# Kernel optimization log

Measured on AMD Instinct MI355X. Metric: run time of the kernel, lower is better.

Reference implementation:

```python
import jax, jax.numpy as jnp
import numpy as np

COUNT_BINS = 8
BOUND = 3.0
MIN_BIN_WIDTH = 1e-3
MIN_BIN_HEIGHT = 1e-3
MIN_DERIVATIVE = 1e-3
EPS = 1e-6


def _made_masks(D, H1, H2, M):
    indeg = np.arange(1, D + 1)                     # input degrees 1..D
    h1 = np.arange(H1) % (D - 1) + 1                # hidden degrees in [1, D-1]
    h2 = np.arange(H2) % (D - 1) + 1
    outdeg = np.tile(indeg, M)                      # (M*D,), reshape-compatible with (M, D)
    m1 = (h1[:, None] >= indeg[None, :]).astype(np.float32)   # (H1, D)
    m2 = (h2[:, None] >= h1[None, :]).astype(np.float32)      # (H2, H1)
    m3 = (outdeg[:, None] > h2[None, :]).astype(np.float32)   # (M*D, H2)
    return jnp.asarray(m1), jnp.asarray(m2), jnp.asarray(m3)


def _rq_spline_forward(x, w, h, d):
    # x: (B, D); w, h: (B, D, K) simplex weights; d: (B, D, K-1) softplus'd interior derivatives
    K = w.shape[-1]
    left, right = -BOUND, BOUND

    widths = MIN_BIN_WIDTH + (1.0 - MIN_BIN_WIDTH * K) * w
    heights = MIN_BIN_HEIGHT + (1.0 - MIN_BIN_HEIGHT * K) * h
    derivs = MIN_DERIVATIVE + d
    ones = jnp.ones_like(derivs[..., :1])
    derivs = jnp.concatenate([ones, derivs, ones], -1)          # (B, D, K+1), boundary slope 1

    cw = jnp.cumsum(widths, -1)
    edge_l = jnp.full_like(cw[..., :1], left)
    edge_r = jnp.full_like(cw[..., :1], right)
    cumw = jnp.concatenate([edge_l, left + (right - left) * cw[..., :-1], edge_r], -1)  # (B, D, K+1)
    widths = cumw[..., 1:] - cumw[..., :-1]
    ch = jnp.cumsum(heights, -1)
    cumh = jnp.concatenate([edge_l, left + (right - left) * ch[..., :-1], edge_r], -1)
    heights = cumh[..., 1:] - cumh[..., :-1]

    inside = (x >= left) & (x <= right)
    xc = jnp.clip(x, left, right)
    # pyro: bin_idx = sum(x >= cumwidths + eps) - 1
    idx = jnp.sum((xc[..., None] >= (cumw + EPS)).astype(jnp.int32), -1) - 1
    idx = jnp.clip(idx, 0, K - 1)                               # (B, D)

    def g(t):
        return jnp.take_along_axis(t, idx[..., None], axis=-1)[..., 0]

    x_k, w_k = g(cumw), g(widths)
    y_k, h_k = g(cumh), g(heights)
    delta = h_k / w_k
    d_k, d_k1 = g(derivs), g(derivs[..., 1:])

    theta = (xc - x_k) / w_k
    tt = theta * (1.0 - theta)
    num = h_k * (delta * theta ** 2 + d_k * tt)
    den = delta + (d_k + d_k1 - 2.0 * delta) * tt
    y = y_k + num / den
    dnum = delta ** 2 * (d_k1 * theta ** 2 + 2.0 * delta * tt + d_k * (1.0 - theta) ** 2)
    ld = jnp.log(dnum) - 2.0 * jnp.log(den)
    return jnp.where(inside, y, x), jnp.where(inside, ld, jnp.zeros_like(ld))


def _forward(x, W1, b1, W2, b2, W3, b3):
    B, D = x.shape
    H1, H2 = W1.shape[0], W2.shape[0]
    K = COUNT_BINS
    M = 3 * K - 1
    m1, m2, m3 = _made_masks(D, H1, H2, M)
    h1 = jax.nn.relu(x @ (W1 * m1).T + b1)
    h2 = jax.nn.relu(h1 @ (W2 * m2).T + b2)
    p = (h2 @ (W3 * m3).T + b3).reshape(B, M, D)                # (B, 3K-1, D)
    w = jax.nn.softmax(jnp.swapaxes(p[:, :K, :], 1, 2), axis=-1)          # (B, D, K)
    hgt = jax.nn.softmax(jnp.swapaxes(p[:, K:2 * K, :], 1, 2), axis=-1)   # (B, D, K)
    d = jax.nn.softplus(jnp.swapaxes(p[:, 2 * K:, :], 1, 2))              # (B, D, K-1)
    z, ld = _rq_spline_forward(x, w, hgt, d)
    return z, ld.sum(-1)


def setup_inputs() -> dict:
    key = jax.random.key(0)
    ks = jax.random.split(key, 7)
    B, D, H1, H2 = 32768, 64, 64, 32
    M = 3 * COUNT_BINS - 1
    s1, s2, s3 = 1.0 / np.sqrt(D), 1.0 / np.sqrt(H1), 1.0 / np.sqrt(H2)
    return {
        "x": jax.random.normal(ks[0], (B, D), jnp.float32),
        "W1": jax.random.uniform(ks[1], (H1, D), jnp.float32, -s1, s1),
        "b1": jax.random.uniform(ks[2], (H1,), jnp.float32, -s1, s1),
        "W2": jax.random.uniform(ks[3], (H2, H1), jnp.float32, -s2, s2),
        "b2": jax.random.uniform(ks[4], (H2,), jnp.float32, -s2, s2),
        "W3": jax.random.uniform(ks[5], (M * D, H2), jnp.float32, -s3, s3),
        "b3": jax.random.uniform(ks[6], (M * D,), jnp.float32, -s3, s3),
    }


def reference(x, W1, b1, W2, b2, W3, b3):
    return _forward(x, W1, b1, W2, b2, W3, b3)
```

## Files before the change

kernel.cpp:

```cpp
#include <hip/hip_runtime.h>

#define NM 23

typedef short short8 __attribute__((ext_vector_type(8)));
typedef float f32x4 __attribute__((ext_vector_type(4)));

__device__ __forceinline__ float softplus_f(float v) {
  return fmaxf(v, 0.f) + __logf(1.f + __expf(-fabsf(v)));
}

__device__ __forceinline__ float fastrcp(float v) {
  return __builtin_amdgcn_rcpf(v);
}

__device__ __forceinline__ unsigned short bf16_rne(float x) {
  unsigned u = __float_as_uint(x);
  u += 0x7FFFu + ((u >> 16) & 1u);
  return (unsigned short)(u >> 16);
}

__global__ __launch_bounds__(256) void prep_kernel(
    const float* __restrict__ W1, const float* __restrict__ W2,
    const float* __restrict__ W3,
    unsigned short* __restrict__ B1hi, unsigned short* __restrict__ B1lo,
    unsigned short* __restrict__ B2hi, unsigned short* __restrict__ B2lo,
    unsigned short* __restrict__ B3hi, unsigned short* __restrict__ B3lo) {
  const int idx = blockIdx.x * 256 + threadIdx.x;
  const int j = idx & 7, lane = (idx >> 3) & 63;
  const int col = lane & 15, quad = lane >> 4;

  if (idx < 4096) {
    const int rest = idx >> 9, kt = rest & 1, nt = rest >> 1;
    const int k = kt * 32 + quad * 8 + j;
    const int n = nt * 16 + col;
    const float v = ((n % 63) >= k) ? W1[n * 64 + k] : 0.f;
    const unsigned short h = bf16_rne(v);
    B1hi[idx] = h;
    B1lo[idx] = bf16_rne(v - __uint_as_float(((unsigned)h) << 16));
  }
  if (idx < 2048) {
    const int rest = idx >> 9, kt = rest & 1, nt = rest >> 1;
    const int k = kt * 32 + quad * 8 + j;
    const int n = nt * 16 + col;
    const float v = ((k % 63) <= n) ? W2[n * 64 + k] : 0.f;
    const unsigned short h = bf16_rne(v);
    B2hi[idx] = h;
    B2lo[idx] = bf16_rne(v - __uint_as_float(((unsigned)h) << 16));
  }
  if (idx < 92 * 64 * 8) {
    const int nt = idx >> 9;
    const int n = nt * 16 + col;
    const int d = n & 63;
    const int k = quad * 8 + j;
    const float v = (k < d) ? W3[(size_t)n * 32 + k] : 0.f;
    const unsigned short h = bf16_rne(v);
    B3hi[idx] = h;
    B3lo[idx] = bf16_rne(v - __uint_as_float(((unsigned)h) << 16));
  }
}

__device__ __forceinline__ void cvt_hilo(const float* src, short8& hi,
                                         short8& lo) {
  const f32x4 a0 = *reinterpret_cast<const f32x4*>(src);
  const f32x4 a1 = *reinterpret_cast<const f32x4*>(src + 4);
  const float af[8] = {a0.x, a0.y, a0.z, a0.w, a1.x, a1.y, a1.z, a1.w};
  #pragma unroll
  for (int j = 0; j < 8; ++j) {
    const unsigned short h = bf16_rne(af[j]);
    hi[j] = (short)h;
    lo[j] = (short)bf16_rne(af[j] - __uint_as_float(((unsigned)h) << 16));
  }
}

__global__ __launch_bounds__(256, 2) void fused_kernel(
    const float* __restrict__ x,
    const unsigned short* __restrict__ B1hi,
    const unsigned short* __restrict__ B1lo,
    const float* __restrict__ b1,
    const unsigned short* __restrict__ B2hi,
    const unsigned short* __restrict__ B2lo,
    const float* __restrict__ b2,
    const unsigned short* __restrict__ B3hi,
    const unsigned short* __restrict__ B3lo,
    const float* __restrict__ b3,
    float* __restrict__ out, int B) {
  __shared__ float xs[64][68];
  __shared__ float h1s[64][68];
  __shared__ float h2s[64][36];
  __shared__ float b3s[64 * NM];

  const int t = threadIdx.x;
  const int b0 = blockIdx.x * 64;

  #pragma unroll
  for (int u = 0; u < 4; ++u) {
    const int idx = t + u * 256;
    const int rr = idx >> 4, c4 = (idx & 15) * 4;
    const float4 v = *reinterpret_cast<const float4*>(
        x + (size_t)b0 * 64 + (size_t)idx * 4);
    xs[rr][c4 + 0] = v.x; xs[rr][c4 + 1] = v.y;
    xs[rr][c4 + 2] = v.z; xs[rr][c4 + 3] = v.w;
  }
  for (int idx = t; idx < 64 * NM; idx += 256) {
    const int dl = idx / NM, m = idx - dl * NM;
    b3s[idx] = b3[m * 64 + dl];
  }
  __syncthreads();

  const int lane = t & 63;
  const int wv   = __builtin_amdgcn_readfirstlane(t >> 6);
  const int mt   = wv;
  const int col  = lane & 15;
  const int quad = lane >> 4;
  const int arow = mt * 16 + col;

  {
    short8 ahi[2], alo[2];
    #pragma unroll
    for (int kt = 0; kt < 2; ++kt)
      cvt_hilo(&xs[arow][kt * 32 + quad * 8], ahi[kt], alo[kt]);

    #pragma unroll
    for (int nt = 0; nt < 4; ++nt) {
      const float bv = b1[nt * 16 + col];
      f32x4 acc = {bv, bv, bv, bv};
      #pragma unroll
      for (int kt = 0; kt < 2; ++kt) {
        const size_t off = ((size_t)(nt * 2 + kt) * 64 + lane) * 8;
        const short8 bh = *reinterpret_cast<const short8*>(B1hi + off);
        const short8 bl = *reinterpret_cast<const short8*>(B1lo + off);
        acc = __builtin_amdgcn_mfma_f32_16x16x32_bf16(ahi[kt], bh, acc, 0, 0, 0);
        acc = __builtin_amdgcn_mfma_f32_16x16x32_bf16(alo[kt], bh, acc, 0, 0, 0);
        acc = __builtin_amdgcn_mfma_f32_16x16x32_bf16(ahi[kt], bl, acc, 0, 0, 0);
      }
      #pragma unroll
      for (int reg = 0; reg < 4; ++reg)
        h1s[mt * 16 + quad * 4 + reg][nt * 16 + col] = fmaxf(acc[reg], 0.f);
    }
  }

  {
    short8 ahi[2], alo[2];
    #pragma unroll
    for (int kt = 0; kt < 2; ++kt)
      cvt_hilo(&h1s[arow][kt * 32 + quad * 8], ahi[kt], alo[kt]);

    #pragma unroll
    for (int nt = 0; nt < 2; ++nt) {
      const float bv = b2[nt * 16 + col];
      f32x4 acc = {bv, bv, bv, bv};
      #pragma unroll
      for (int kt = 0; kt < 2; ++kt) {
        const size_t off = ((size_t)(nt * 2 + kt) * 64 + lane) * 8;
        const short8 bh = *reinterpret_cast<const short8*>(B2hi + off);
        const short8 bl = *reinterpret_cast<const short8*>(B2lo + off);
        acc = __builtin_amdgcn_mfma_f32_16x16x32_bf16(ahi[kt], bh, acc, 0, 0, 0);
        acc = __builtin_amdgcn_mfma_f32_16x16x32_bf16(alo[kt], bh, acc, 0, 0, 0);
        acc = __builtin_amdgcn_mfma_f32_16x16x32_bf16(ahi[kt], bl, acc, 0, 0, 0);
      }
      #pragma unroll
      for (int reg = 0; reg < 4; ++reg)
        h2s[mt * 16 + quad * 4 + reg][nt * 16 + col] = fmaxf(acc[reg], 0.f);
    }
  }

  short8 ahi, alo;
  cvt_hilo(&h2s[arow][quad * 8], ahi, alo);

  float ldr[4] = {0.f, 0.f, 0.f, 0.f};

  #pragma unroll 1
  for (int jj = 0; jj < 4; ++jj) {
    const int dc = jj;
    const int d  = dc * 16 + col;

    f32x4 acc[NM];
    #pragma unroll
    for (int m = 0; m < NM; ++m) {
      const float bv = b3s[d * NM + m];
      acc[m] = (f32x4){bv, bv, bv, bv};
    }
    #pragma unroll
    for (int m = 0; m < NM; ++m) {
      const int nt = 4 * m + dc;
      const size_t off = ((size_t)nt * 64 + lane) * 8;
      const short8 bh = *reinterpret_cast<const short8*>(B3hi + off);
      const short8 bl = *reinterpret_cast<const short8*>(B3lo + off);
      acc[m] = __builtin_amdgcn_mfma_f32_16x16x32_bf16(ahi, bh, acc[m], 0, 0, 0);
      acc[m] = __builtin_amdgcn_mfma_f32_16x16x32_bf16(alo, bh, acc[m], 0, 0, 0);
      acc[m] = __builtin_amdgcn_mfma_f32_16x16x32_bf16(ahi, bl, acc[m], 0, 0, 0);
    }

    #pragma unroll
    for (int reg = 0; reg < 4; ++reg) {
      const int row = mt * 16 + quad * 4 + reg;

      float p[NM];
      #pragma unroll
      for (int m = 0; m < NM; ++m) p[m] = acc[m][reg];

      const float xv = xs[row][d];
      const float xc = fminf(fmaxf(xv, -3.f), 3.f);

      float ew[8], sw = 0.f;
      #pragma unroll
      for (int k = 0; k < 8; ++k) { ew[k] = __expf(p[k]); sw += ew[k]; }
      const float invw = fastrcp(sw);

      float eh[8], sh = 0.f;
      #pragma unroll
      for (int k = 0; k < 8; ++k) { eh[k] = __expf(p[8 + k]); sh += eh[k]; }
      const float invh = fastrcp(sh);

      const float WSC = 1.0f - 1e-3f * 8.0f;
      float cumw[9], cumh[9];
      cumw[0] = -3.f; cumh[0] = -3.f;
      float cw = 0.f, ch = 0.f;
      #pragma unroll
      for (int k = 0; k < 7; ++k) {
        cw += 1e-3f + WSC * (ew[k] * invw);
        ch += 1e-3f + WSC * (eh[k] * invh);
        cumw[k + 1] = fmaf(6.f, cw, -3.f);
        cumh[k + 1] = fmaf(6.f, ch, -3.f);
      }
      cumw[8] = 3.f; cumh[8] = 3.f;

      float derivs[9];
      derivs[0] = 1.f; derivs[8] = 1.f;
      #pragma unroll
      for (int k = 0; k < 7; ++k) derivs[k + 1] = 1e-3f + softplus_f(p[16 + k]);

      float xk = cumw[0], xk1 = cumw[1];
      float yk = cumh[0], yk1 = cumh[1];
      float dk = derivs[0], dk1 = derivs[1];
      #pragma unroll
      for (int k = 1; k < 8; ++k) {
        const bool s = xc >= cumw[k] + 1e-6f;
        xk  = s ? cumw[k]       : xk;
        xk1 = s ? cumw[k + 1]   : xk1;
        yk  = s ? cumh[k]       : yk;
        yk1 = s ? cumh[k + 1]   : yk1;
        dk  = s ? derivs[k]     : dk;
        dk1 = s ? derivs[k + 1] : dk1;
      }

      const float wk = xk1 - xk, hk = yk1 - yk;
      const float invwk = fastrcp(wk);
      const float delta = hk * invwk;
      const float theta = (xc - xk) * invwk;
      const float omt = 1.f - theta;
      const float tt = theta * omt;
      const float th2 = theta * theta;
      const float num = hk * (delta * th2 + dk * tt);
      const float den = delta + (dk + dk1 - 2.f * delta) * tt;
      const float rden = fastrcp(den);
      const float yv = yk + num * rden;
      const float dnum = delta * delta * (dk1 * th2 + 2.f * delta * tt + dk * omt * omt);
      const float ldv = __logf(dnum * rden * rden);

      const bool inside = (xv >= -3.f) && (xv <= 3.f);
      xs[row][d] = inside ? yv : xv;
      ldr[reg] += inside ? ldv : 0.f;
    }
  }

  #pragma unroll
  for (int mask = 1; mask <= 8; mask <<= 1) {
    #pragma unroll
    for (int reg = 0; reg < 4; ++reg)
      ldr[reg] += __shfl_xor(ldr[reg], mask, 64);
  }
  __syncthreads();

  if (col == 0) {
    #pragma unroll
    for (int reg = 0; reg < 4; ++reg)
      out[(size_t)B * 64 + b0 + mt * 16 + quad * 4 + reg] = ldr[reg];
  }

  #pragma unroll
  for (int u = 0; u < 4; ++u) {
    const int idx = t + u * 256;
    const int rr = idx >> 4, c4 = (idx & 15) * 4;
    const float4 v = make_float4(xs[rr][c4 + 0], xs[rr][c4 + 1],
                                 xs[rr][c4 + 2], xs[rr][c4 + 3]);
    *reinterpret_cast<float4*>(out + (size_t)(b0 + rr) * 64 + c4) = v;
  }
}

extern "C" void kernel_launch(void* const* d_in, const int* in_sizes, int n_in,
                              void* d_out, int out_size, void* d_ws, size_t ws_size,
                              hipStream_t stream) {
  const float* x  = (const float*)d_in[0];
  const float* W1 = (const float*)d_in[1];
  const float* b1 = (const float*)d_in[2];
  const float* W2 = (const float*)d_in[3];
  const float* b2 = (const float*)d_in[4];
  const float* W3 = (const float*)d_in[5];
  const float* b3 = (const float*)d_in[6];
  float* out = (float*)d_out;
  char* ws   = (char*)d_ws;

  unsigned short* B1hi = (unsigned short*)(ws);
  unsigned short* B1lo = (unsigned short*)(ws + 8192);
  unsigned short* B2hi = (unsigned short*)(ws + 16384);
  unsigned short* B2lo = (unsigned short*)(ws + 20480);
  unsigned short* B3hi = (unsigned short*)(ws + 24576);
  unsigned short* B3lo = (unsigned short*)(ws + 118784);

  const int B = in_sizes[0] / 64;

  prep_kernel<<<184, 256, 0, stream>>>(W1, W2, W3, B1hi, B1lo, B2hi, B2lo,
                                       B3hi, B3lo);

  fused_kernel<<<B / 64, 256, 0, stream>>>(
      x, B1hi, B1lo, b1, B2hi, B2lo, b2, B3hi, B3lo, b3, out, B);
}
```

Measured before the change: 118.4 us.

## Split layer-3 MFMA into three phases to cut registers and raise occupancy

Removes the shared-memory staging tile for x and z, reading x straight from global memory and writing z directly with strided scalar stores. The 23-accumulator layer-3 GEMM is split into three phases (widths, heights, derivatives), each followed by its part of the spline math, so far fewer accumulator registers are live at once. The launch bound is raised to 4 blocks per SIMD. Costs: uncoalesced global loads and stores of x/z, a bin-index carried as float, and a select-based derivative gather.

```diff
diff --git a/kernel.cpp b/kernel.cpp
--- a/kernel.cpp
+++ b/kernel.cpp
@@ -72,7 +72,7 @@
   }
 }
 
-__global__ __launch_bounds__(256, 2) void fused_kernel(
+__global__ __launch_bounds__(256, 4) void fused_kernel(
     const float* __restrict__ x,
     const unsigned short* __restrict__ B1hi,
     const unsigned short* __restrict__ B1lo,
@@ -84,7 +84,6 @@
     const unsigned short* __restrict__ B3lo,
     const float* __restrict__ b3,
     float* __restrict__ out, int B) {
-  __shared__ float xs[64][68];
   __shared__ float h1s[64][68];
   __shared__ float h2s[64][36];
   __shared__ float b3s[64 * NM];
@@ -92,15 +91,6 @@
   const int t = threadIdx.x;
   const int b0 = blockIdx.x * 64;
 
-  #pragma unroll
-  for (int u = 0; u < 4; ++u) {
-    const int idx = t + u * 256;
-    const int rr = idx >> 4, c4 = (idx & 15) * 4;
-    const float4 v = *reinterpret_cast<const float4*>(
-        x + (size_t)b0 * 64 + (size_t)idx * 4);
-    xs[rr][c4 + 0] = v.x; xs[rr][c4 + 1] = v.y;
-    xs[rr][c4 + 2] = v.z; xs[rr][c4 + 3] = v.w;
-  }
   for (int idx = t; idx < 64 * NM; idx += 256) {
     const int dl = idx / NM, m = idx - dl * NM;
     b3s[idx] = b3[m * 64 + dl];
@@ -115,10 +105,11 @@
   const int arow = mt * 16 + col;
 
   {
+    const float* xrow = x + (size_t)(b0 + arow) * 64;
     short8 ahi[2], alo[2];
     #pragma unroll
     for (int kt = 0; kt < 2; ++kt)
-      cvt_hilo(&xs[arow][kt * 32 + quad * 8], ahi[kt], alo[kt]);
+      cvt_hilo(xrow + kt * 32 + quad * 8, ahi[kt], alo[kt]);
 
     #pragma unroll
     for (int nt = 0; nt < 4; ++nt) {
@@ -168,99 +159,165 @@
   cvt_hilo(&h2s[arow][quad * 8], ahi, alo);
 
   float ldr[4] = {0.f, 0.f, 0.f, 0.f};
+  const float* xg = x + (size_t)b0 * 64;
+  float* zg = out + (size_t)b0 * 64;
+  const int row0 = mt * 16 + quad * 4;
+  const float WSC = 1.0f - 1e-3f * 8.0f;
 
   #pragma unroll 1
-  for (int jj = 0; jj < 4; ++jj) {
-    const int dc = jj;
-    const int d  = dc * 16 + col;
-
-    f32x4 acc[NM];
-    #pragma unroll
-    for (int m = 0; m < NM; ++m) {
-      const float bv = b3s[d * NM + m];
-      acc[m] = (f32x4){bv, bv, bv, bv};
-    }
-    #pragma unroll
-    for (int m = 0; m < NM; ++m) {
-      const int nt = 4 * m + dc;
-      const size_t off = ((size_t)nt * 64 + lane) * 8;
-      const short8 bh = *reinterpret_cast<const short8*>(B3hi + off);
-      const short8 bl = *reinterpret_cast<const short8*>(B3lo + off);
-      acc[m] = __builtin_amdgcn_mfma_f32_16x16x32_bf16(ahi, bh, acc[m], 0, 0, 0);
-      acc[m] = __builtin_amdgcn_mfma_f32_16x16x32_bf16(alo, bh, acc[m], 0, 0, 0);
-      acc[m] = __builtin_amdgcn_mfma_f32_16x16x32_bf16(ahi, bl, acc[m], 0, 0, 0);
-    }
-
-    #pragma unroll
-    for (int reg = 0; reg < 4; ++reg) {
-      const int row = mt * 16 + quad * 4 + reg;
-
-      float p[NM];
-      #pragma unroll
-      for (int m = 0; m < NM; ++m) p[m] = acc[m][reg];
-
-      const float xv = xs[row][d];
-      const float xc = fminf(fmaxf(xv, -3.f), 3.f);
-
-      float ew[8], sw = 0.f;
-      #pragma unroll
-      for (int k = 0; k < 8; ++k) { ew[k] = __expf(p[k]); sw += ew[k]; }
-      const float invw = fastrcp(sw);
-
-      float eh[8], sh = 0.f;
-      #pragma unroll
-      for (int k = 0; k < 8; ++k) { eh[k] = __expf(p[8 + k]); sh += eh[k]; }
-      const float invh = fastrcp(sh);
-
-      const float WSC = 1.0f - 1e-3f * 8.0f;
-      float cumw[9], cumh[9];
-      cumw[0] = -3.f; cumh[0] = -3.f;
-      float cw = 0.f, ch = 0.f;
-      #pragma unroll
-      for (int k = 0; k < 7; ++k) {
-        cw += 1e-3f + WSC * (ew[k] * invw);
-        ch += 1e-3f + WSC * (eh[k] * invh);
-        cumw[k + 1] = fmaf(6.f, cw, -3.f);
-        cumh[k + 1] = fmaf(6.f, ch, -3.f);
-      }
-      cumw[8] = 3.f; cumh[8] = 3.f;
-
-      float derivs[9];
-      derivs[0] = 1.f; derivs[8] = 1.f;
-      #pragma unroll
-      for (int k = 0; k < 7; ++k) derivs[k + 1] = 1e-3f + softplus_f(p[16 + k]);
-
-      float xk = cumw[0], xk1 = cumw[1];
-      float yk = cumh[0], yk1 = cumh[1];
-      float dk = derivs[0], dk1 = derivs[1];
-      #pragma unroll
-      for (int k = 1; k < 8; ++k) {
-        const bool s = xc >= cumw[k] + 1e-6f;
-        xk  = s ? cumw[k]       : xk;
-        xk1 = s ? cumw[k + 1]   : xk1;
-        yk  = s ? cumh[k]       : yk;
-        yk1 = s ? cumh[k + 1]   : yk1;
-        dk  = s ? derivs[k]     : dk;
-        dk1 = s ? derivs[k + 1] : dk1;
-      }
-
-      const float wk = xk1 - xk, hk = yk1 - yk;
-      const float invwk = fastrcp(wk);
-      const float delta = hk * invwk;
-      const float theta = (xc - xk) * invwk;
-      const float omt = 1.f - theta;
-      const float tt = theta * omt;
-      const float th2 = theta * theta;
-      const float num = hk * (delta * th2 + dk * tt);
-      const float den = delta + (dk + dk1 - 2.f * delta) * tt;
-      const float rden = fastrcp(den);
-      const float yv = yk + num * rden;
-      const float dnum = delta * delta * (dk1 * th2 + 2.f * delta * tt + dk * omt * omt);
-      const float ldv = __logf(dnum * rden * rden);
-
-      const bool inside = (xv >= -3.f) && (xv <= 3.f);
-      xs[row][d] = inside ? yv : xv;
-      ldr[reg] += inside ? ldv : 0.f;
+  for (int dc = 0; dc < 4; ++dc) {
+    const int d = dc * 16 + col;
+
+    float xvv[4];
+    #pragma unroll
+    for (int reg = 0; reg < 4; ++reg)
+      xvv[reg] = xg[(size_t)(row0 + reg) * 64 + d];
+
+    float xcv[4], fidx[4], xkv[4], wkv[4], ykv[4], hkv[4];
+
+    {
+      f32x4 acc[8];
+      #pragma unroll
+      for (int m = 0; m < 8; ++m) {
+        const float bv = b3s[d * NM + m];
+        acc[m] = (f32x4){bv, bv, bv, bv};
+      }
+      #pragma unroll
+      for (int m = 0; m < 8; ++m) {
+        const size_t off = ((size_t)(4 * m + dc) * 64 + lane) * 8;
+        const short8 bh = *reinterpret_cast<const short8*>(B3hi + off);
+        const short8 bl = *reinterpret_cast<const short8*>(B3lo + off);
+        acc[m] = __builtin_amdgcn_mfma_f32_16x16x32_bf16(ahi, bh, acc[m], 0, 0, 0);
+        acc[m] = __builtin_amdgcn_mfma_f32_16x16x32_bf16(alo, bh, acc[m], 0, 0, 0);
+        acc[m] = __builtin_amdgcn_mfma_f32_16x16x32_bf16(ahi, bl, acc[m], 0, 0, 0);
+      }
+      #pragma unroll
+      for (int reg = 0; reg < 4; ++reg) {
+        float ew[8], sw = 0.f;
+        #pragma unroll
+        for (int k = 0; k < 8; ++k) { ew[k] = __expf(acc[k][reg]); sw += ew[k]; }
+        const float invw = fastrcp(sw);
+        float cumw[9];
+        cumw[0] = -3.f;
+        float cw = 0.f;
+        #pragma unroll
+        for (int k = 0; k < 7; ++k) {
+          cw += 1e-3f + WSC * (ew[k] * invw);
+          cumw[k + 1] = fmaf(6.f, cw, -3.f);
+        }
+        cumw[8] = 3.f;
+
+        const float xv = xvv[reg];
+        const float xc = fminf(fmaxf(xv, -3.f), 3.f);
+        float fi = 0.f, xk = cumw[0], xk1 = cumw[1];
+        #pragma unroll
+        for (int k = 1; k < 8; ++k) {
+          const bool s = xc >= cumw[k] + 1e-6f;
+          xk  = s ? cumw[k]     : xk;
+          xk1 = s ? cumw[k + 1] : xk1;
+          fi  = s ? (float)k    : fi;
+        }
+        xcv[reg] = xc; fidx[reg] = fi; xkv[reg] = xk; wkv[reg] = xk1 - xk;
+      }
+    }
+
+    {
+      f32x4 acc[8];
+      #pragma unroll
+      for (int m = 0; m < 8; ++m) {
+        const float bv = b3s[d * NM + (8 + m)];
+        acc[m] = (f32x4){bv, bv, bv, bv};
+      }
+      #pragma unroll
+      for (int m = 0; m < 8; ++m) {
+        const size_t off = ((size_t)(4 * (8 + m) + dc) * 64 + lane) * 8;
+        const short8 bh = *reinterpret_cast<const short8*>(B3hi + off);
+        const short8 bl = *reinterpret_cast<const short8*>(B3lo + off);
+        acc[m] = __builtin_amdgcn_mfma_f32_16x16x32_bf16(ahi, bh, acc[m], 0, 0, 0);
+        acc[m] = __builtin_amdgcn_mfma_f32_16x16x32_bf16(alo, bh, acc[m], 0, 0, 0);
+        acc[m] = __builtin_amdgcn_mfma_f32_16x16x32_bf16(ahi, bl, acc[m], 0, 0, 0);
+      }
+      #pragma unroll
+      for (int reg = 0; reg < 4; ++reg) {
+        float eh[8], sh = 0.f;
+        #pragma unroll
+        for (int k = 0; k < 8; ++k) { eh[k] = __expf(acc[k][reg]); sh += eh[k]; }
+        const float invh = fastrcp(sh);
+        float cumh[9];
+        cumh[0] = -3.f;
+        float ch = 0.f;
+        #pragma unroll
+        for (int k = 0; k < 7; ++k) {
+          ch += 1e-3f + WSC * (eh[k] * invh);
+          cumh[k + 1] = fmaf(6.f, ch, -3.f);
+        }
+        cumh[8] = 3.f;
+
+        float yk = cumh[0], yk1 = cumh[1];
+        #pragma unroll
+        for (int k = 1; k < 8; ++k) {
+          const bool s = fidx[reg] >= (float)k;
+          yk  = s ? cumh[k]     : yk;
+          yk1 = s ? cumh[k + 1] : yk1;
+        }
+        ykv[reg] = yk; hkv[reg] = yk1 - yk;
+      }
+    }
+
+    {
+      f32x4 acc[7];
+      #pragma unroll
+      for (int m = 0; m < 7; ++m) {
+        const float bv = b3s[d * NM + (16 + m)];
+        acc[m] = (f32x4){bv, bv, bv, bv};
+      }
+      #pragma unroll
+      for (int m = 0; m < 7; ++m) {
+        const size_t off = ((size_t)(4 * (16 + m) + dc) * 64 + lane) * 8;
+        const short8 bh = *reinterpret_cast<const short8*>(B3hi + off);
+        const short8 bl = *reinterpret_cast<const short8*>(B3lo + off);
+        acc[m] = __builtin_amdgcn_mfma_f32_16x16x32_bf16(ahi, bh, acc[m], 0, 0, 0);
+        acc[m] = __builtin_amdgcn_mfma_f32_16x16x32_bf16(alo, bh, acc[m], 0, 0, 0);
+        acc[m] = __builtin_amdgcn_mfma_f32_16x16x32_bf16(ahi, bl, acc[m], 0, 0, 0);
+      }
+      #pragma unroll
+      for (int reg = 0; reg < 4; ++reg) {
+        float p[7];
+        #pragma unroll
+        for (int k = 0; k < 7; ++k) p[k] = acc[k][reg];
+        const float fi = fidx[reg];
+
+        float pa = p[0], pb = p[0];
+        #pragma unroll
+        for (int k = 2; k < 8; ++k) pa = (fi >= (float)k) ? p[k - 1] : pa;
+        #pragma unroll
+        for (int k = 1; k < 7; ++k) pb = (fi >= (float)k) ? p[k] : pb;
+        const float spa = 1e-3f + softplus_f(pa);
+        const float spb = 1e-3f + softplus_f(pb);
+        const float dk  = (fi >= 0.5f) ? spa : 1.f;
+        const float dk1 = (fi >= 6.5f) ? 1.f : spb;
+
+        const float xc = xcv[reg], xk = xkv[reg], wk = wkv[reg];
+        const float yk = ykv[reg], hk = hkv[reg];
+        const float invwk = fastrcp(wk);
+        const float delta = hk * invwk;
+        const float theta = (xc - xk) * invwk;
+        const float omt = 1.f - theta;
+        const float tt = theta * omt;
+        const float th2 = theta * theta;
+        const float num = hk * (delta * th2 + dk * tt);
+        const float den = delta + (dk + dk1 - 2.f * delta) * tt;
+        const float rden = fastrcp(den);
+        const float yv = yk + num * rden;
+        const float dnum =
+            delta * delta * (dk1 * th2 + 2.f * delta * tt + dk * omt * omt);
+        const float ldv = __logf(dnum * rden * rden);
+
+        const float xv = xvv[reg];
+        const bool inside = (xv >= -3.f) && (xv <= 3.f);
+        zg[(size_t)(row0 + reg) * 64 + d] = inside ? yv : xv;
+        ldr[reg] += inside ? ldv : 0.f;
+      }
     }
   }
 
@@ -270,21 +327,11 @@
     for (int reg = 0; reg < 4; ++reg)
       ldr[reg] += __shfl_xor(ldr[reg], mask, 64);
   }
-  __syncthreads();
 
   if (col == 0) {
     #pragma unroll
     for (int reg = 0; reg < 4; ++reg)
-      out[(size_t)B * 64 + b0 + mt * 16 + quad * 4 + reg] = ldr[reg];
-  }
-
-  #pragma unroll
-  for (int u = 0; u < 4; ++u) {
-    const int idx = t + u * 256;
-    const int rr = idx >> 4, c4 = (idx & 15) * 4;
-    const float4 v = make_float4(xs[rr][c4 + 0], xs[rr][c4 + 1],
-                                 xs[rr][c4 + 2], xs[rr][c4 + 3]);
-    *reinterpret_cast<float4*>(out + (size_t)(b0 + rr) * 64 + c4) = v;
+      out[(size_t)B * 64 + b0 + row0 + reg] = ldr[reg];
   }
 }
 
```

Measured after the change: 118.2 us. Within noise of the previous version (-0.2%).
